# Optimization experiments

Measured on AMD Instinct MI355X. Metric: run time of the kernel, lower is better.

## Reference

```python
import jax, jax.numpy as jnp
import numpy as np

B, N_MAX, H, STEPS = 8, 36, 64, 5


def setup_inputs() -> dict:
    key = jax.random.key(0)
    ks = jax.random.split(key, 6)
    bound = 1.0 / np.sqrt(H)
    return {
        "edge_wgt": jax.random.normal(ks[0], (B, N_MAX, N_MAX, H, H), dtype=jnp.float32) * 0.1,
        "nodes_embed": jax.random.normal(ks[1], (B, N_MAX, H), dtype=jnp.float32),
        "mask": jnp.ones((B, N_MAX, 1), dtype=jnp.float32),
        "w_ih": jax.random.uniform(ks[2], (3 * H, H), jnp.float32, -bound, bound),
        "w_hh": jax.random.uniform(ks[3], (3 * H, H), jnp.float32, -bound, bound),
        "b_ih": jax.random.uniform(ks[4], (3 * H,), jnp.float32, -bound, bound),
        "b_hh": jax.random.uniform(ks[5], (3 * H,), jnp.float32, -bound, bound),
    }


def _gru_cell(x, h, w_ih, w_hh, b_ih, b_hh):
    # torch.nn.GRUCell math; x, h: [..., H]
    gi = x @ w_ih.T + b_ih
    gh = h @ w_hh.T + b_hh
    i_r, i_z, i_n = jnp.split(gi, 3, axis=-1)
    h_r, h_z, h_n = jnp.split(gh, 3, axis=-1)
    r = jax.nn.sigmoid(i_r + h_r)
    z = jax.nn.sigmoid(i_z + h_z)
    n = jnp.tanh(i_n + r * h_n)
    return (1.0 - z) * n + z * h


def reference(edge_wgt, nodes_embed, mask, w_ih, w_hh, b_ih, b_hh):
    n_max = edge_wgt.shape[1]
    inv_n2 = 1.0 / (n_max * n_max)
    nodes = nodes_embed
    for _ in range(STEPS):
        # messages[b,j,k] = (1/n^2) * sum_{i,l} edge_wgt[b,i,j,k,l] * nodes[b,i,l]
        messages = jnp.einsum('bijkl,bil->bjk', edge_wgt, nodes) * inv_n2
        nodes = _gru_cell(messages, nodes, w_ih, w_hh, b_ih, b_hh) * mask
    return nodes
```

## Files before the change

### kernel.cpp

```cpp
#include <hip/hip_runtime.h>
#include <hip/hip_bf16.h>


#define BB 8
#define NN 36
#define HH 64
#define WAVES 4
#define IPW (NN / WAVES)
#define NBJ (BB * NN)
#define INVN2 (1.0f / (float)(NN * NN))

typedef unsigned u32x4 __attribute__((ext_vector_type(4)));

__device__ __forceinline__ unsigned pack_bf16_2(float lo, float hi) {
    __hip_bfloat16 a = __float2bfloat16(lo);
    __hip_bfloat16 b = __float2bfloat16(hi);
    unsigned ua = *reinterpret_cast<unsigned short*>(&a);
    unsigned ub = *reinterpret_cast<unsigned short*>(&b);
    return ua | (ub << 16);
}

__device__ __forceinline__ float gru_lane(
    const float* __restrict__ ms, const float* __restrict__ hs, int t,
    const float* __restrict__ w_ih, const float* __restrict__ w_hh,
    const float* __restrict__ b_ih, const float* __restrict__ b_hh)
{
    float gi0 = b_ih[t], gi1 = b_ih[HH + t], gi2 = b_ih[2 * HH + t];
    float gh0 = b_hh[t], gh1 = b_hh[HH + t], gh2 = b_hh[2 * HH + t];

    const float4* __restrict__ wi0 = (const float4*)(w_ih + (0 * HH + t) * HH);
    const float4* __restrict__ wi1 = (const float4*)(w_ih + (1 * HH + t) * HH);
    const float4* __restrict__ wi2 = (const float4*)(w_ih + (2 * HH + t) * HH);
    const float4* __restrict__ wh0 = (const float4*)(w_hh + (0 * HH + t) * HH);
    const float4* __restrict__ wh1 = (const float4*)(w_hh + (1 * HH + t) * HH);
    const float4* __restrict__ wh2 = (const float4*)(w_hh + (2 * HH + t) * HH);

    #pragma unroll
    for (int k4 = 0; k4 < HH / 4; ++k4) {
        const float4 mv = *(const float4*)&ms[k4 * 4];
        const float4 hv = *(const float4*)&hs[k4 * 4];
        float4 a;
        a = wi0[k4]; gi0 += a.x * mv.x + a.y * mv.y + a.z * mv.z + a.w * mv.w;
        a = wi1[k4]; gi1 += a.x * mv.x + a.y * mv.y + a.z * mv.z + a.w * mv.w;
        a = wi2[k4]; gi2 += a.x * mv.x + a.y * mv.y + a.z * mv.z + a.w * mv.w;
        a = wh0[k4]; gh0 += a.x * hv.x + a.y * hv.y + a.z * hv.z + a.w * hv.w;
        a = wh1[k4]; gh1 += a.x * hv.x + a.y * hv.y + a.z * hv.z + a.w * hv.w;
        a = wh2[k4]; gh2 += a.x * hv.x + a.y * hv.y + a.z * hv.z + a.w * hv.w;
    }
    const float r = 1.f / (1.f + expf(-(gi0 + gh0)));
    const float z = 1.f / (1.f + expf(-(gi1 + gh1)));
    const float n = tanhf(gi2 + r * gh2);
    return (1.f - z) * n + z * hs[t];
}

__global__ __launch_bounds__(64) void einsum_f32_cvt(
    const float* __restrict__ edge,
    const float* __restrict__ nodes,
    float* __restrict__ partial,
    u32x4* __restrict__ ebf)
{
    const int lane = threadIdx.x;
    const int bid  = blockIdx.x;
    const int j = bid % NN;
    const int i = (bid / NN) % NN;
    const int b = bid / (NN * NN);

    const int p = lane & 7;
    const int q = lane >> 3;

    const float* np_ = nodes + (b * NN + i) * HH + p * 8;
    const float4 v0 = *(const float4*)(np_);
    const float4 v1 = *(const float4*)(np_ + 4);

    const size_t blkElem = (size_t)((b * NN + i) * NN + j) * (HH * HH);
    const float* __restrict__ Wf = edge + blkElem;
    u32x4* __restrict__ Eb = ebf + (blkElem >> 3);

    float acc[8];
    #pragma unroll
    for (int it = 0; it < 8; ++it) acc[it] = 0.f;

    #pragma unroll
    for (int it = 0; it < 8; ++it) {
        const int o = it * 64 + lane;
        const float4 a = *(const float4*)(Wf + (size_t)o * 8);
        const float4 c = *(const float4*)(Wf + (size_t)o * 8 + 4);
        acc[it] = fmaf(a.x, v0.x, acc[it]);
        acc[it] = fmaf(a.y, v0.y, acc[it]);
        acc[it] = fmaf(a.z, v0.z, acc[it]);
        acc[it] = fmaf(a.w, v0.w, acc[it]);
        acc[it] = fmaf(c.x, v1.x, acc[it]);
        acc[it] = fmaf(c.y, v1.y, acc[it]);
        acc[it] = fmaf(c.z, v1.z, acc[it]);
        acc[it] = fmaf(c.w, v1.w, acc[it]);
        u32x4 pk;
        pk.x = pack_bf16_2(a.x, a.y);
        pk.y = pack_bf16_2(a.z, a.w);
        pk.z = pack_bf16_2(c.x, c.y);
        pk.w = pack_bf16_2(c.z, c.w);
        Eb[o] = pk;
    }

    #pragma unroll
    for (int m = 1; m < 8; m <<= 1) {
        #pragma unroll
        for (int it = 0; it < 8; ++it)
            acc[it] += __shfl_xor(acc[it], m, 64);
    }

    float outv = acc[0];
    #pragma unroll
    for (int t = 1; t < 8; ++t) outv = (p == t) ? acc[t] : outv;

    partial[((size_t)(b * NN + j) * NN + i) * HH + (8 * p + q)] = outv;
}

__global__ __launch_bounds__(64) void gru_step(
    const float* __restrict__ partial,
    const float* __restrict__ nodes_in,
    const float* __restrict__ mask,
    const float* __restrict__ w_ih, const float* __restrict__ w_hh,
    const float* __restrict__ b_ih, const float* __restrict__ b_hh,
    float* __restrict__ nodes_out)
{
    const int t  = threadIdx.x;
    const int bj = blockIdx.x;

    const float* pp = partial + (size_t)bj * NN * HH;
    float m = 0.f;
    #pragma unroll
    for (int i = 0; i < NN; ++i)
        m += pp[i * HH + t];

    __shared__ float ms[HH];
    __shared__ float hs[HH];
    ms[t] = m * INVN2;
    hs[t] = nodes_in[bj * HH + t];
    __syncthreads();

    const float o = gru_lane(ms, hs, t, w_ih, w_hh, b_ih, b_hh);
    nodes_out[bj * HH + t] = o * mask[bj];
}

__global__ __launch_bounds__(256, 2) void step_bf16(
    const uint4* __restrict__ ebf,
    const float* __restrict__ nodes_in,
    const float* __restrict__ mask,
    const float* __restrict__ w_ih, const float* __restrict__ w_hh,
    const float* __restrict__ b_ih, const float* __restrict__ b_hh,
    float* __restrict__ nodes_out)
{
    const int tid  = threadIdx.x;
    const int lane = tid & 63;
    const int wv   = tid >> 6;
    const int bj = blockIdx.x;
    const int j  = bj % NN;
    const int b  = bj / NN;

    __shared__ float part[WAVES][HH];
    __shared__ float ms[HH];
    __shared__ float hs[HH];

    const int l8 = lane & 7;

    float acc[8];
    #pragma unroll
    for (int it = 0; it < 8; ++it) acc[it] = 0.f;

    for (int ii = 0; ii < IPW; ++ii) {
        const int i = wv * IPW + ii;
        const float* np_ = nodes_in + (b * NN + i) * HH + l8 * 8;
        const float4 v0 = *(const float4*)(np_);
        const float4 v1 = *(const float4*)(np_ + 4);
        const size_t blkElem = (size_t)((b * NN + i) * NN + j) * (HH * HH);
        const uint4* __restrict__ Wb = ebf + (blkElem >> 3);
        #pragma unroll
        for (int it = 0; it < 8; ++it) {
            const uint4 w = Wb[it * 64 + lane];
            acc[it] = fmaf(__uint_as_float(w.x << 16),          v0.x, acc[it]);
            acc[it] = fmaf(__uint_as_float(w.x & 0xffff0000u),  v0.y, acc[it]);
            acc[it] = fmaf(__uint_as_float(w.y << 16),          v0.z, acc[it]);
            acc[it] = fmaf(__uint_as_float(w.y & 0xffff0000u),  v0.w, acc[it]);
            acc[it] = fmaf(__uint_as_float(w.z << 16),          v1.x, acc[it]);
            acc[it] = fmaf(__uint_as_float(w.z & 0xffff0000u),  v1.y, acc[it]);
            acc[it] = fmaf(__uint_as_float(w.w << 16),          v1.z, acc[it]);
            acc[it] = fmaf(__uint_as_float(w.w & 0xffff0000u),  v1.w, acc[it]);
        }
    }

    #pragma unroll
    for (int m = 1; m < 8; m <<= 1) {
        #pragma unroll
        for (int it = 0; it < 8; ++it)
            acc[it] += __shfl_xor(acc[it], m, 64);
    }

    const int p  = lane & 7;
    const int gq = lane >> 3;
    float outv = acc[0];
    #pragma unroll
    for (int tt = 1; tt < 8; ++tt) outv = (p == tt) ? acc[tt] : outv;
    part[wv][8 * p + gq] = outv;

    __syncthreads();

    if (tid < HH) {
        const float m = part[0][tid] + part[1][tid] + part[2][tid] + part[3][tid];
        ms[tid] = m * INVN2;
        hs[tid] = nodes_in[bj * HH + tid];
    }
    __syncthreads();

    if (tid < HH) {
        const float o = gru_lane(ms, hs, tid, w_ih, w_hh, b_ih, b_hh);
        nodes_out[bj * HH + tid] = o * mask[bj];
    }
}

extern "C" void kernel_launch(void* const* d_in, const int* in_sizes, int n_in,
                              void* d_out, int out_size, void* d_ws, size_t ws_size,
                              hipStream_t stream) {
    const float* edge   = (const float*)d_in[0];
    const float* nodes0 = (const float*)d_in[1];
    const float* mask   = (const float*)d_in[2];
    const float* w_ih   = (const float*)d_in[3];
    const float* w_hh   = (const float*)d_in[4];
    const float* b_ih   = (const float*)d_in[5];
    const float* b_hh   = (const float*)d_in[6];
    float* out = (float*)d_out;

    float* ws = (float*)d_ws;
    const int nodes_elems   = BB * NN * HH;
    const int partial_elems = NBJ * NN * HH;
    float* nodesA  = ws;
    float* nodesB  = ws + nodes_elems;
    float* partial = ws + 2 * nodes_elems;
    float* ebf_f   = partial + partial_elems;
    u32x4* ebf4w = (u32x4*)ebf_f;
    const uint4* ebf4 = (const uint4*)ebf_f;

    einsum_f32_cvt<<<BB * NN * NN, 64, 0, stream>>>(edge, nodes0, partial, ebf4w);
    gru_step<<<NBJ, 64, 0, stream>>>(partial, nodes0, mask,
                                     w_ih, w_hh, b_ih, b_hh, nodesA);
    step_bf16<<<NBJ, 256, 0, stream>>>(ebf4, nodesA, mask,
                                       w_ih, w_hh, b_ih, b_hh, nodesB);
    step_bf16<<<NBJ, 256, 0, stream>>>(ebf4, nodesB, mask,
                                       w_ih, w_hh, b_ih, b_hh, nodesA);
    step_bf16<<<NBJ, 256, 0, stream>>>(ebf4, nodesA, mask,
                                       w_ih, w_hh, b_ih, b_hh, nodesB);
    step_bf16<<<NBJ, 256, 0, stream>>>(ebf4, nodesB, mask,
                                       w_ih, w_hh, b_ih, b_hh, out);
}
```

Measured before the change: 145.5 us.

## Pipeline stages across batches in a wavefront of fused mega-kernel launches

Replaces the six sequential launches (full fp32 einsum plus bf16 convert, GRU, four bf16 steps) with one multi-role kernel launched 13 times. Each launch runs a different stage for each of several batches at once: convert for batch t, GRU for batch t-1, and bf16 steps for batches t-2..t-5. The intent is to overlap the bandwidth-heavy fp32 read of one batch with the smaller, latency-bound recurrent steps of earlier batches, so the GPU stays busy instead of idling on small step grids. The cost is more launches (13 instead of 6), branchy block-role dispatch, and each per-batch convert stage using only 324 blocks.

```diff
diff --git a/kernel.cpp b/kernel.cpp
--- a/kernel.cpp
+++ b/kernel.cpp
@@ -5,8 +5,6 @@
 #define BB 8
 #define NN 36
 #define HH 64
-#define WAVES 4
-#define IPW (NN / WAVES)
 #define NBJ (BB * NN)
 #define INVN2 (1.0f / (float)(NN * NN))
 
@@ -53,167 +51,177 @@
     return (1.f - z) * n + z * hs[t];
 }
 
-__global__ __launch_bounds__(64) void einsum_f32_cvt(
+__global__ __launch_bounds__(256, 2) void mega(
     const float* __restrict__ edge,
-    const float* __restrict__ nodes,
+    u32x4* __restrict__ ebf_w, const uint4* __restrict__ ebf_r,
     float* __restrict__ partial,
-    u32x4* __restrict__ ebf)
-{
-    const int lane = threadIdx.x;
-    const int bid  = blockIdx.x;
-    const int j = bid % NN;
-    const int i = (bid / NN) % NN;
-    const int b = bid / (NN * NN);
-
-    const int p = lane & 7;
-    const int q = lane >> 3;
-
-    const float* np_ = nodes + (b * NN + i) * HH + p * 8;
-    const float4 v0 = *(const float4*)(np_);
-    const float4 v1 = *(const float4*)(np_ + 4);
-
-    const size_t blkElem = (size_t)((b * NN + i) * NN + j) * (HH * HH);
-    const float* __restrict__ Wf = edge + blkElem;
-    u32x4* __restrict__ Eb = ebf + (blkElem >> 3);
-
-    float acc[8];
-    #pragma unroll
-    for (int it = 0; it < 8; ++it) acc[it] = 0.f;
-
-    #pragma unroll
-    for (int it = 0; it < 8; ++it) {
-        const int o = it * 64 + lane;
-        const float4 a = *(const float4*)(Wf + (size_t)o * 8);
-        const float4 c = *(const float4*)(Wf + (size_t)o * 8 + 4);
-        acc[it] = fmaf(a.x, v0.x, acc[it]);
-        acc[it] = fmaf(a.y, v0.y, acc[it]);
-        acc[it] = fmaf(a.z, v0.z, acc[it]);
-        acc[it] = fmaf(a.w, v0.w, acc[it]);
-        acc[it] = fmaf(c.x, v1.x, acc[it]);
-        acc[it] = fmaf(c.y, v1.y, acc[it]);
-        acc[it] = fmaf(c.z, v1.z, acc[it]);
-        acc[it] = fmaf(c.w, v1.w, acc[it]);
-        u32x4 pk;
-        pk.x = pack_bf16_2(a.x, a.y);
-        pk.y = pack_bf16_2(a.z, a.w);
-        pk.z = pack_bf16_2(c.x, c.y);
-        pk.w = pack_bf16_2(c.z, c.w);
-        Eb[o] = pk;
-    }
-
-    #pragma unroll
-    for (int m = 1; m < 8; m <<= 1) {
-        #pragma unroll
-        for (int it = 0; it < 8; ++it)
-            acc[it] += __shfl_xor(acc[it], m, 64);
-    }
-
-    float outv = acc[0];
-    #pragma unroll
-    for (int t = 1; t < 8; ++t) outv = (p == t) ? acc[t] : outv;
-
-    partial[((size_t)(b * NN + j) * NN + i) * HH + (8 * p + q)] = outv;
-}
-
-__global__ __launch_bounds__(64) void gru_step(
-    const float* __restrict__ partial,
-    const float* __restrict__ nodes_in,
+    const float* __restrict__ nodes0,
     const float* __restrict__ mask,
     const float* __restrict__ w_ih, const float* __restrict__ w_hh,
     const float* __restrict__ b_ih, const float* __restrict__ b_hh,
-    float* __restrict__ nodes_out)
+    int cvt_b,
+    int gru_b, float* __restrict__ gru_out,
+    int sb0, const float* __restrict__ sin0, float* __restrict__ sout0,
+    int sb1, const float* __restrict__ sin1, float* __restrict__ sout1,
+    int sb2, const float* __restrict__ sin2, float* __restrict__ sout2,
+    int sb3, const float* __restrict__ sin3, float* __restrict__ sout3)
 {
-    const int t  = threadIdx.x;
-    const int bj = blockIdx.x;
-
-    const float* pp = partial + (size_t)bj * NN * HH;
-    float m = 0.f;
-    #pragma unroll
-    for (int i = 0; i < NN; ++i)
-        m += pp[i * HH + t];
-
-    __shared__ float ms[HH];
-    __shared__ float hs[HH];
-    ms[t] = m * INVN2;
-    hs[t] = nodes_in[bj * HH + t];
-    __syncthreads();
-
-    const float o = gru_lane(ms, hs, t, w_ih, w_hh, b_ih, b_hh);
-    nodes_out[bj * HH + t] = o * mask[bj];
-}
-
-__global__ __launch_bounds__(256, 2) void step_bf16(
-    const uint4* __restrict__ ebf,
-    const float* __restrict__ nodes_in,
-    const float* __restrict__ mask,
-    const float* __restrict__ w_ih, const float* __restrict__ w_hh,
-    const float* __restrict__ b_ih, const float* __restrict__ b_hh,
-    float* __restrict__ nodes_out)
-{
+    int blk = blockIdx.x;
     const int tid  = threadIdx.x;
     const int lane = tid & 63;
     const int wv   = tid >> 6;
-    const int bj = blockIdx.x;
-    const int j  = bj % NN;
-    const int b  = bj / NN;
-
-    __shared__ float part[WAVES][HH];
-    __shared__ float ms[HH];
-    __shared__ float hs[HH];
-
-    const int l8 = lane & 7;
-
-    float acc[8];
-    #pragma unroll
-    for (int it = 0; it < 8; ++it) acc[it] = 0.f;
-
-    for (int ii = 0; ii < IPW; ++ii) {
-        const int i = wv * IPW + ii;
-        const float* np_ = nodes_in + (b * NN + i) * HH + l8 * 8;
-        const float4 v0 = *(const float4*)(np_);
-        const float4 v1 = *(const float4*)(np_ + 4);
-        const size_t blkElem = (size_t)((b * NN + i) * NN + j) * (HH * HH);
-        const uint4* __restrict__ Wb = ebf + (blkElem >> 3);
+
+    if (cvt_b >= 0) {
+        if (blk < 324) {
+            const int tile = blk * 4 + wv;
+            const int i = tile / NN;
+            const int j = tile % NN;
+            const int b = cvt_b;
+
+            const int p = lane & 7;
+            const int q = lane >> 3;
+
+            const float* np_ = nodes0 + (b * NN + i) * HH + p * 8;
+            const float4 v0 = *(const float4*)(np_);
+            const float4 v1 = *(const float4*)(np_ + 4);
+
+            const size_t blkElem = (size_t)((b * NN + i) * NN + j) * (HH * HH);
+            const float* __restrict__ Wf = edge + blkElem;
+            u32x4* __restrict__ Eb = ebf_w + (blkElem >> 3);
+
+            float acc[8];
+            #pragma unroll
+            for (int it = 0; it < 8; ++it) acc[it] = 0.f;
+
+            #pragma unroll
+            for (int it = 0; it < 8; ++it) {
+                const int o = it * 64 + lane;
+                const float4 a = *(const float4*)(Wf + (size_t)o * 8);
+                const float4 c = *(const float4*)(Wf + (size_t)o * 8 + 4);
+                acc[it] = fmaf(a.x, v0.x, acc[it]);
+                acc[it] = fmaf(a.y, v0.y, acc[it]);
+                acc[it] = fmaf(a.z, v0.z, acc[it]);
+                acc[it] = fmaf(a.w, v0.w, acc[it]);
+                acc[it] = fmaf(c.x, v1.x, acc[it]);
+                acc[it] = fmaf(c.y, v1.y, acc[it]);
+                acc[it] = fmaf(c.z, v1.z, acc[it]);
+                acc[it] = fmaf(c.w, v1.w, acc[it]);
+                u32x4 pk;
+                pk.x = pack_bf16_2(a.x, a.y);
+                pk.y = pack_bf16_2(a.z, a.w);
+                pk.z = pack_bf16_2(c.x, c.y);
+                pk.w = pack_bf16_2(c.z, c.w);
+                Eb[o] = pk;
+            }
+
+            #pragma unroll
+            for (int m = 1; m < 8; m <<= 1) {
+                #pragma unroll
+                for (int it = 0; it < 8; ++it)
+                    acc[it] += __shfl_xor(acc[it], m, 64);
+            }
+
+            float outv = acc[0];
+            #pragma unroll
+            for (int t = 1; t < 8; ++t) outv = (p == t) ? acc[t] : outv;
+
+            partial[((size_t)(b * NN + j) * NN + i) * HH + (8 * p + q)] = outv;
+            return;
+        }
+        blk -= 324;
+    }
+
+    if (gru_b >= 0) {
+        if (blk < 9) {
+            __shared__ float gms[4][HH];
+            __shared__ float ghs[4][HH];
+            const int node = blk * 4 + wv;
+            const int bj = gru_b * NN + node;
+            const float* pp = partial + (size_t)bj * NN * HH;
+            float m = 0.f;
+            #pragma unroll
+            for (int i = 0; i < NN; ++i)
+                m += pp[i * HH + lane];
+            gms[wv][lane] = m * INVN2;
+            ghs[wv][lane] = nodes0[bj * HH + lane];
+            __syncthreads();
+            const float o = gru_lane(gms[wv], ghs[wv], lane, w_ih, w_hh, b_ih, b_hh);
+            gru_out[bj * HH + lane] = o * mask[bj];
+            return;
+        }
+        blk -= 9;
+    }
+
+    int sb = -1; const float* sin = nullptr; float* sout = nullptr;
+    if (sb0 >= 0) { if (blk < 36) { sb = sb0; sin = sin0; sout = sout0; } else blk -= 36; }
+    if (sb < 0 && sb1 >= 0) { if (blk < 36) { sb = sb1; sin = sin1; sout = sout1; } else blk -= 36; }
+    if (sb < 0 && sb2 >= 0) { if (blk < 36) { sb = sb2; sin = sin2; sout = sout2; } else blk -= 36; }
+    if (sb < 0 && sb3 >= 0) { if (blk < 36) { sb = sb3; sin = sin3; sout = sout3; } else blk -= 36; }
+    if (sb < 0) return;
+
+    {
+        const int j  = blk;
+        const int b  = sb;
+        const int bj = b * NN + j;
+
+        __shared__ float part[4][HH];
+        __shared__ float ms[HH];
+        __shared__ float hs[HH];
+
+        const int l8 = lane & 7;
+
+        float acc[8];
         #pragma unroll
-        for (int it = 0; it < 8; ++it) {
-            const uint4 w = Wb[it * 64 + lane];
-            acc[it] = fmaf(__uint_as_float(w.x << 16),          v0.x, acc[it]);
-            acc[it] = fmaf(__uint_as_float(w.x & 0xffff0000u),  v0.y, acc[it]);
-            acc[it] = fmaf(__uint_as_float(w.y << 16),          v0.z, acc[it]);
-            acc[it] = fmaf(__uint_as_float(w.y & 0xffff0000u),  v0.w, acc[it]);
-            acc[it] = fmaf(__uint_as_float(w.z << 16),          v1.x, acc[it]);
-            acc[it] = fmaf(__uint_as_float(w.z & 0xffff0000u),  v1.y, acc[it]);
-            acc[it] = fmaf(__uint_as_float(w.w << 16),          v1.z, acc[it]);
-            acc[it] = fmaf(__uint_as_float(w.w & 0xffff0000u),  v1.w, acc[it]);
-        }
-    }
-
-    #pragma unroll
-    for (int m = 1; m < 8; m <<= 1) {
+        for (int it = 0; it < 8; ++it) acc[it] = 0.f;
+
+        for (int ii = 0; ii < 9; ++ii) {
+            const int i = wv * 9 + ii;
+            const float* np_ = sin + (b * NN + i) * HH + l8 * 8;
+            const float4 v0 = *(const float4*)(np_);
+            const float4 v1 = *(const float4*)(np_ + 4);
+            const size_t blkElem = (size_t)((b * NN + i) * NN + j) * (HH * HH);
+            const uint4* __restrict__ Wb = ebf_r + (blkElem >> 3);
+            #pragma unroll
+            for (int it = 0; it < 8; ++it) {
+                const uint4 w = Wb[it * 64 + lane];
+                acc[it] = fmaf(__uint_as_float(w.x << 16),          v0.x, acc[it]);
+                acc[it] = fmaf(__uint_as_float(w.x & 0xffff0000u),  v0.y, acc[it]);
+                acc[it] = fmaf(__uint_as_float(w.y << 16),          v0.z, acc[it]);
+                acc[it] = fmaf(__uint_as_float(w.y & 0xffff0000u),  v0.w, acc[it]);
+                acc[it] = fmaf(__uint_as_float(w.z << 16),          v1.x, acc[it]);
+                acc[it] = fmaf(__uint_as_float(w.z & 0xffff0000u),  v1.y, acc[it]);
+                acc[it] = fmaf(__uint_as_float(w.w << 16),          v1.z, acc[it]);
+                acc[it] = fmaf(__uint_as_float(w.w & 0xffff0000u),  v1.w, acc[it]);
+            }
+        }
+
         #pragma unroll
-        for (int it = 0; it < 8; ++it)
-            acc[it] += __shfl_xor(acc[it], m, 64);
-    }
-
-    const int p  = lane & 7;
-    const int gq = lane >> 3;
-    float outv = acc[0];
-    #pragma unroll
-    for (int tt = 1; tt < 8; ++tt) outv = (p == tt) ? acc[tt] : outv;
-    part[wv][8 * p + gq] = outv;
-
-    __syncthreads();
-
-    if (tid < HH) {
-        const float m = part[0][tid] + part[1][tid] + part[2][tid] + part[3][tid];
-        ms[tid] = m * INVN2;
-        hs[tid] = nodes_in[bj * HH + tid];
-    }
-    __syncthreads();
-
-    if (tid < HH) {
-        const float o = gru_lane(ms, hs, tid, w_ih, w_hh, b_ih, b_hh);
-        nodes_out[bj * HH + tid] = o * mask[bj];
+        for (int m = 1; m < 8; m <<= 1) {
+            #pragma unroll
+            for (int it = 0; it < 8; ++it)
+                acc[it] += __shfl_xor(acc[it], m, 64);
+        }
+
+        const int p  = lane & 7;
+        const int gq = lane >> 3;
+        float outv = acc[0];
+        #pragma unroll
+        for (int tt = 1; tt < 8; ++tt) outv = (p == tt) ? acc[tt] : outv;
+        part[wv][8 * p + gq] = outv;
+
+        __syncthreads();
+
+        if (tid < HH) {
+            const float m = part[0][tid] + part[1][tid] + part[2][tid] + part[3][tid];
+            ms[tid] = m * INVN2;
+            hs[tid] = sin[bj * HH + tid];
+        }
+        __syncthreads();
+
+        if (tid < HH) {
+            const float o = gru_lane(ms, hs, tid, w_ih, w_hh, b_ih, b_hh);
+            sout[bj * HH + tid] = o * mask[bj];
+        }
     }
 }
 
@@ -230,24 +238,49 @@
     float* out = (float*)d_out;
 
     float* ws = (float*)d_ws;
-    const int nodes_elems   = BB * NN * HH;
-    const int partial_elems = NBJ * NN * HH;
-    float* nodesA  = ws;
-    float* nodesB  = ws + nodes_elems;
-    float* partial = ws + 2 * nodes_elems;
-    float* ebf_f   = partial + partial_elems;
-    u32x4* ebf4w = (u32x4*)ebf_f;
-    const uint4* ebf4 = (const uint4*)ebf_f;
-
-    einsum_f32_cvt<<<BB * NN * NN, 64, 0, stream>>>(edge, nodes0, partial, ebf4w);
-    gru_step<<<NBJ, 64, 0, stream>>>(partial, nodes0, mask,
-                                     w_ih, w_hh, b_ih, b_hh, nodesA);
-    step_bf16<<<NBJ, 256, 0, stream>>>(ebf4, nodesA, mask,
-                                       w_ih, w_hh, b_ih, b_hh, nodesB);
-    step_bf16<<<NBJ, 256, 0, stream>>>(ebf4, nodesB, mask,
-                                       w_ih, w_hh, b_ih, b_hh, nodesA);
-    step_bf16<<<NBJ, 256, 0, stream>>>(ebf4, nodesA, mask,
-                                       w_ih, w_hh, b_ih, b_hh, nodesB);
-    step_bf16<<<NBJ, 256, 0, stream>>>(ebf4, nodesB, mask,
-                                       w_ih, w_hh, b_ih, b_hh, out);
-}
+    const int nodes_elems   = NBJ * HH;
+    const size_t partial_elems = (size_t)NBJ * NN * HH;
+    float* partial = ws;
+    float* n1 = ws + partial_elems;
+    float* n2 = n1 + nodes_elems;
+    float* n3 = n2 + nodes_elems;
+    float* n4 = n3 + nodes_elems;
+    float* ebf_f = n4 + nodes_elems;
+    u32x4* ebf_w = (u32x4*)ebf_f;
+    const uint4* ebf_r = (const uint4*)ebf_f;
+
+    float* nin[6];
+    nin[2] = n1; nin[3] = n2; nin[4] = n3; nin[5] = n4;
+    float* nout[6];
+    nout[2] = n2; nout[3] = n3; nout[4] = n4; nout[5] = out;
+
+    for (int t = 0; t < 13; ++t) {
+        const int cvt_b = (t < BB) ? t : -1;
+        const int gru_b = (t - 1 >= 0 && t - 1 < BB) ? (t - 1) : -1;
+        int sb[4] = {-1, -1, -1, -1};
+        const float* sin[4] = {nullptr, nullptr, nullptr, nullptr};
+        float* sout[4] = {nullptr, nullptr, nullptr, nullptr};
+        int nblk = 0;
+        if (cvt_b >= 0) nblk += 324;
+        if (gru_b >= 0) nblk += 9;
+        for (int s = 2; s <= 5; ++s) {
+            const int b = t - s;
+            const int slot = s - 2;
+            if (b >= 0 && b < BB) {
+                sb[slot] = b;
+                sin[slot] = nin[s];
+                sout[slot] = nout[s];
+                nblk += 36;
+            }
+        }
+        if (nblk == 0) continue;
+        mega<<<nblk, 256, 0, stream>>>(
+            edge, ebf_w, ebf_r, partial, nodes0, mask,
+            w_ih, w_hh, b_ih, b_hh,
+            cvt_b, gru_b, n1,
+            sb[0], sin[0], sout[0],
+            sb[1], sin[1], sout[1],
+            sb[2], sin[2], sout[2],
+            sb[3], sin[3], sout[3]);
+    }
+}
```

New measurement: 213.2 us. +46.5%, slower.
